# Kernel optimization log

Measured on AMD Instinct MI355X. Metric: run time of the kernel, lower is better.

## Reference

```python
import jax, jax.numpy as jnp
import numpy as np

D_MODEL = 1024
N_HEADS = 16
D_K = D_MODEL // N_HEADS
CAUSAL = True


def setup_inputs() -> dict:
    key = jax.random.key(0)
    ks = jax.random.split(key, 11)
    B, S, D = 2, 2048, D_MODEL
    scale = 1.0 / np.sqrt(D)
    inp = {
        "in_Q": jax.random.normal(ks[0], (B, S, D), jnp.float32),
        "in_K": jax.random.normal(ks[1], (B, S, D), jnp.float32),
        "in_V": jax.random.normal(ks[2], (B, S, D), jnp.float32),
        # torch Linear params: weight [out, in], bias [out]
        "Wq": jax.random.normal(ks[3], (D, D), jnp.float32) * scale,
        "bq": jax.random.normal(ks[4], (D,), jnp.float32) * scale,
        "Wk": jax.random.normal(ks[5], (D, D), jnp.float32) * scale,
        "bk": jax.random.normal(ks[6], (D,), jnp.float32) * scale,
        "Wv": jax.random.normal(ks[7], (D, D), jnp.float32) * scale,
        "bv": jax.random.normal(ks[8], (D,), jnp.float32) * scale,
        "Wo": jax.random.normal(ks[9], (D, D), jnp.float32) * scale,
        "bo": jax.random.normal(ks[10], (D,), jnp.float32) * scale,
    }
    return inp


def reference(in_Q, in_K, in_V, Wq, bq, Wk, bk, Wv, bv, Wo, bo):
    B, S, D = in_Q.shape
    H, dk = N_HEADS, D_K
    # Linear projections (torch: x @ W.T + b)
    Q = in_Q @ Wq.T + bq
    K = in_K @ Wk.T + bk
    V = in_V @ Wv.T + bv
    # split heads: [B, S, D] -> [B, H, S, dk]
    Qh = Q.reshape(B, S, H, dk).transpose(0, 2, 1, 3)
    Kh = K.reshape(B, S, H, dk).transpose(0, 2, 1, 3)
    Vh = V.reshape(B, S, H, dk).transpose(0, 2, 1, 3)
    # scores [B, H, S, S]
    scores = jnp.einsum("bhqd,bhkd->bhqk", Qh, Kh) / jnp.sqrt(jnp.float32(dk))
    if CAUSAL:
        mask = jnp.tril(jnp.ones((S, S), dtype=bool))
        scores = jnp.where(mask, scores, -jnp.inf)
    attn = jax.nn.softmax(scores, axis=-1)
    out = jnp.einsum("bhqk,bhkd->bhqd", attn, Vh)
    Hcat = out.transpose(0, 2, 1, 3).reshape(B, S, D)
    return Hcat @ Wo.T + bo
```

## Files before the change

### kernel.cpp

```cpp
#include <hip/hip_runtime.h>
#include <hip/hip_bf16.h>
#include <math.h>

#define D_MODEL 1024
#define NHEADS  16
#define DK      64
#define SEQ     2048
#define BATCH   2
#define MROWS   4096

typedef unsigned short ushort_t;
using short8 = __attribute__((ext_vector_type(8))) short;
using f32x4  = __attribute__((ext_vector_type(4))) float;

__device__ __forceinline__ ushort_t f2bf(float x) {
    unsigned u = __float_as_uint(x);
    u = (u + 0x7FFFu + ((u >> 16) & 1u)) >> 16;
    return (ushort_t)u;
}

__device__ __forceinline__ unsigned pk2(float a, float b) {
    __hip_bfloat162 h = __float22bfloat162_rn(float2{a, b});
    unsigned u;
    __builtin_memcpy(&u, &h, 4);
    return u;
}

__device__ __forceinline__ void gll16(const ushort_t* g, ushort_t* l) {
    __builtin_amdgcn_global_load_lds(
        (const __attribute__((address_space(1))) void*)(g),
        (__attribute__((address_space(3))) void*)(l), 16, 0, 0);
}

__global__ __launch_bounds__(256) void cvt_bf16(
    const float* s0, const float* s1, const float* s2, const float* s3,
    ushort_t* d0, ushort_t* d1, ushort_t* d2, ushort_t* d3, int n)
{
    const float* s; ushort_t* d;
    switch (blockIdx.y) {
        case 0: s = s0; d = d0; break;
        case 1: s = s1; d = d1; break;
        case 2: s = s2; d = d2; break;
        default: s = s3; d = d3; break;
    }
    int i = (blockIdx.x * 256 + threadIdx.x) * 4;
    if (i < n) {
        float4 v = *(const float4*)&s[i];
        ushort4 o;
        o.x = f2bf(v.x); o.y = f2bf(v.y); o.z = f2bf(v.z); o.w = f2bf(v.w);
        *(ushort4*)&d[i] = o;
    }
}

struct GemmArgs { const ushort_t* A; const ushort_t* W; const float* bias;
                  void* C; int mode; float oscale; };

template<int MODE>
__device__ __forceinline__ void gemm_core(const GemmArgs& ga,
                                          ushort_t* As, ushort_t* Bs)
{
    constexpr bool SWP = (MODE != 1);
    const int tid  = threadIdx.x;
    const int w    = tid >> 6, lane = tid & 63;
    const int quad = lane >> 4, lx = lane & 15;
    const int mw = (w >> 1) * 64, nw = (w & 1) * 64;
    const int bm = blockIdx.x * 128, bn = blockIdx.y * 128;
    const int K = D_MODEL;

    f32x4 acc[4][4];
#pragma unroll
    for (int mt = 0; mt < 4; ++mt)
#pragma unroll
        for (int nt = 0; nt < 4; ++nt)
            acc[mt][nt] = (f32x4){0.f, 0.f, 0.f, 0.f};

    float4 b4[4];
    float  bfr[4];
#pragma unroll
    for (int nt = 0; nt < 4; ++nt) {
        if (SWP) b4[nt] = *(const float4*)&ga.bias[bn + nw + nt * 16 + quad * 4];
        else     bfr[nt] = ga.bias[bn + nw + nt * 16 + lx];
    }

    for (int k0 = 0; k0 < K; k0 += 64) {
        __syncthreads();
#pragma unroll
        for (int i = 0; i < 4; ++i) {
            int r0 = (w * 4 + i) * 8;
            int rl = r0 + (lane >> 3);
            int g  = (lane & 7) ^ (rl & 7);
            gll16(&ga.A[(size_t)(bm + rl) * K + k0 + g * 8], &As[r0 * 64]);
            gll16(&ga.W[(size_t)(bn + rl) * K + k0 + g * 8], &Bs[r0 * 64]);
        }
        __syncthreads();

#pragma unroll
        for (int ks = 0; ks < 2; ++ks) {
            short8 af[4], bf[4];
#pragma unroll
            for (int mt = 0; mt < 4; ++mt) {
                int r = mw + mt * 16 + lx;
                af[mt] = *(const short8*)&As[r * 64 + (((ks * 4 + quad) ^ (r & 7)) << 3)];
            }
#pragma unroll
            for (int nt = 0; nt < 4; ++nt) {
                int r = nw + nt * 16 + lx;
                bf[nt] = *(const short8*)&Bs[r * 64 + (((ks * 4 + quad) ^ (r & 7)) << 3)];
            }
#pragma unroll
            for (int mt = 0; mt < 4; ++mt)
#pragma unroll
                for (int nt = 0; nt < 4; ++nt)
                    acc[mt][nt] = SWP
                        ? __builtin_amdgcn_mfma_f32_16x16x32_bf16(bf[nt], af[mt], acc[mt][nt], 0, 0, 0)
                        : __builtin_amdgcn_mfma_f32_16x16x32_bf16(af[mt], bf[nt], acc[mt][nt], 0, 0, 0);
        }
    }

    if (MODE == 0) {
        ushort_t* C = (ushort_t*)ga.C;
        const float os = ga.oscale;
#pragma unroll
        for (int mt = 0; mt < 4; ++mt) {
            int m = bm + mw + mt * 16 + lx;
#pragma unroll
            for (int nt = 0; nt < 4; ++nt) {
                int n0 = bn + nw + nt * 16 + quad * 4;
                uint2 u;
                u.x = pk2((acc[mt][nt][0] + b4[nt].x) * os, (acc[mt][nt][1] + b4[nt].y) * os);
                u.y = pk2((acc[mt][nt][2] + b4[nt].z) * os, (acc[mt][nt][3] + b4[nt].w) * os);
                *(uint2*)&C[(size_t)m * D_MODEL + n0] = u;
            }
        }
    } else if (MODE == 2) {
        float* C = (float*)ga.C;
#pragma unroll
        for (int mt = 0; mt < 4; ++mt) {
            int m = bm + mw + mt * 16 + lx;
#pragma unroll
            for (int nt = 0; nt < 4; ++nt) {
                int n0 = bn + nw + nt * 16 + quad * 4;
                float4 v;
                v.x = acc[mt][nt][0] + b4[nt].x;
                v.y = acc[mt][nt][1] + b4[nt].y;
                v.z = acc[mt][nt][2] + b4[nt].z;
                v.w = acc[mt][nt][3] + b4[nt].w;
                *(float4*)&C[(size_t)m * D_MODEL + n0] = v;
            }
        }
    } else {
        ushort_t* C = (ushort_t*)ga.C;
#pragma unroll
        for (int mt = 0; mt < 4; ++mt)
#pragma unroll
            for (int nt = 0; nt < 4; ++nt) {
                int n = bn + nw + nt * 16 + lx;
                int d = n & 63, h = n >> 6;
                int m0 = bm + mw + mt * 16 + quad * 4;
                int b = m0 >> 11, s0 = m0 & 2047;
                uint2 u;
                u.x = pk2(acc[mt][nt][0] + bfr[nt], acc[mt][nt][1] + bfr[nt]);
                u.y = pk2(acc[mt][nt][2] + bfr[nt], acc[mt][nt][3] + bfr[nt]);
                *(uint2*)&C[((size_t)(b * NHEADS + h) * DK + d) * SEQ + s0] = u;
            }
    }
}

__global__ __launch_bounds__(256) void gemm_mfma(GemmArgs g0, GemmArgs g1, GemmArgs g2)
{
    __shared__ ushort_t As[128 * 64];
    __shared__ ushort_t Bs[128 * 64];
    GemmArgs ga = (blockIdx.z == 0) ? g0 : ((blockIdx.z == 1) ? g1 : g2);
    if (ga.mode == 0)      gemm_core<0>(ga, As, Bs);
    else if (ga.mode == 1) gemm_core<1>(ga, As, Bs);
    else                   gemm_core<2>(ga, As, Bs);
}

__global__ __launch_bounds__(256) void flash_mfma(
    const ushort_t* __restrict__ Qp, const ushort_t* __restrict__ Kp,
    const ushort_t* __restrict__ Vt, ushort_t* __restrict__ Hc)
{
    const int qt = (int)gridDim.x - 1 - (int)blockIdx.x;
    const int bh = blockIdx.y;
    const int b = bh >> 4, h = bh & 15;
    const int tid  = threadIdx.x;
    const int w    = tid >> 6, lane = tid & 63;
    const int quad = lane >> 4, lx = lane & 15;

    __shared__ ushort_t Ks[64 * 64];
    __shared__ ushort_t Vs[64 * 64];
    __shared__ ushort_t Ps[4][16 * 72];

    const size_t qbase = (size_t)(b * SEQ) * D_MODEL + h * DK;
    const size_t vbase = (size_t)bh * DK * SEQ;

    short8 qf[2];
    {
        size_t ro = qbase + (size_t)(qt * 64 + w * 16 + lx) * D_MODEL + quad * 8;
        qf[0] = *(const short8*)&Qp[ro];
        qf[1] = *(const short8*)&Qp[ro + 32];
    }

    f32x4 O[4];
#pragma unroll
    for (int nt = 0; nt < 4; ++nt) O[nt] = (f32x4){0.f, 0.f, 0.f, 0.f};
    float mrow = -INFINITY, lrow = 0.f;
    const int qin = w * 16 + lx;

    for (int kt = 0; kt <= qt; ++kt) {
        __syncthreads();
#pragma unroll
        for (int i = 0; i < 2; ++i) {
            int r0 = (w + i * 4) * 8;
            int rl = r0 + (lane >> 3);
            int g  = (lane & 7) ^ (rl & 7);
            gll16(&Kp[qbase + (size_t)(kt * 64 + rl) * D_MODEL + g * 8], &Ks[r0 * 64]);
            gll16(&Vt[vbase + (size_t)rl * SEQ + kt * 64 + g * 8], &Vs[r0 * 64]);
        }
        __syncthreads();

        f32x4 s[4];
#pragma unroll
        for (int nt = 0; nt < 4; ++nt) {
            int r = nt * 16 + lx;
            short8 kf0 = *(const short8*)&Ks[r * 64 + ((quad ^ (r & 7)) << 3)];
            short8 kf1 = *(const short8*)&Ks[r * 64 + (((4 + quad) ^ (r & 7)) << 3)];
            f32x4 z = (f32x4){0.f, 0.f, 0.f, 0.f};
            z = __builtin_amdgcn_mfma_f32_16x16x32_bf16(kf0, qf[0], z, 0, 0, 0);
            z = __builtin_amdgcn_mfma_f32_16x16x32_bf16(kf1, qf[1], z, 0, 0, 0);
            s[nt] = z;
        }

        if (kt == qt) {
#pragma unroll
            for (int nt = 0; nt < 4; ++nt)
#pragma unroll
                for (int r = 0; r < 4; ++r)
                    if ((nt * 16 + quad * 4 + r) > qin) s[nt][r] = -INFINITY;
        }

        float tm = -INFINITY;
#pragma unroll
        for (int nt = 0; nt < 4; ++nt)
#pragma unroll
            for (int r = 0; r < 4; ++r) tm = fmaxf(tm, s[nt][r]);
        tm = fmaxf(tm, __shfl_xor(tm, 16, 64));
        tm = fmaxf(tm, __shfl_xor(tm, 32, 64));
        float mnew = fmaxf(mrow, tm);
        float alpha = __builtin_amdgcn_exp2f(mrow - mnew);
        mrow = mnew;
        float rs = 0.f;
#pragma unroll
        for (int nt = 0; nt < 4; ++nt)
#pragma unroll
            for (int r = 0; r < 4; ++r) {
                float p = __builtin_amdgcn_exp2f(s[nt][r] - mnew);
                s[nt][r] = p;
                rs += p;
            }
        rs += __shfl_xor(rs, 16, 64);
        rs += __shfl_xor(rs, 32, 64);
        lrow = lrow * alpha + rs;
#pragma unroll
        for (int nt = 0; nt < 4; ++nt)
#pragma unroll
            for (int r = 0; r < 4; ++r) O[nt][r] *= alpha;

#pragma unroll
        for (int nt = 0; nt < 4; ++nt) {
            uint2 u;
            u.x = pk2(s[nt][0], s[nt][1]);
            u.y = pk2(s[nt][2], s[nt][3]);
            *(uint2*)&Ps[w][lx * 72 + nt * 16 + quad * 4] = u;
        }

        short8 pf0 = *(const short8*)&Ps[w][lx * 72 + quad * 8];
        short8 pf1 = *(const short8*)&Ps[w][lx * 72 + 32 + quad * 8];

#pragma unroll
        for (int nt = 0; nt < 4; ++nt) {
            int r = nt * 16 + lx;
            short8 vf0 = *(const short8*)&Vs[r * 64 + ((quad ^ (r & 7)) << 3)];
            short8 vf1 = *(const short8*)&Vs[r * 64 + (((4 + quad) ^ (r & 7)) << 3)];
            O[nt] = __builtin_amdgcn_mfma_f32_16x16x32_bf16(vf0, pf0, O[nt], 0, 0, 0);
            O[nt] = __builtin_amdgcn_mfma_f32_16x16x32_bf16(vf1, pf1, O[nt], 0, 0, 0);
        }
    }

    {
        float invl = 1.f / lrow;
        size_t ro = qbase + (size_t)(qt * 64 + w * 16 + lx) * D_MODEL;
#pragma unroll
        for (int nt = 0; nt < 4; ++nt) {
            uint2 u;
            u.x = pk2(O[nt][0] * invl, O[nt][1] * invl);
            u.y = pk2(O[nt][2] * invl, O[nt][3] * invl);
            *(uint2*)&Hc[ro + nt * 16 + quad * 4] = u;
        }
    }
}

extern "C" void kernel_launch(void* const* d_in, const int* in_sizes, int n_in,
                              void* d_out, int out_size, void* d_ws, size_t ws_size,
                              hipStream_t stream) {
    const float* inQ = (const float*)d_in[0];
    const float* inK = (const float*)d_in[1];
    const float* inV = (const float*)d_in[2];
    const float* Wq  = (const float*)d_in[3];
    const float* bq  = (const float*)d_in[4];
    const float* Wk  = (const float*)d_in[5];
    const float* bk  = (const float*)d_in[6];
    const float* Wv  = (const float*)d_in[7];
    const float* bv  = (const float*)d_in[8];
    const float* Wo  = (const float*)d_in[9];
    const float* bo  = (const float*)d_in[10];
    float* out = (float*)d_out;

    const size_t NI = (size_t)MROWS * D_MODEL;
    const size_t NW = (size_t)D_MODEL * D_MODEL;
    ushort_t* ws  = (ushort_t*)d_ws;
    ushort_t* Qb  = ws;
    ushort_t* Kb  = Qb  + NI;
    ushort_t* Vb  = Kb  + NI;
    ushort_t* Wqb = Vb  + NI;
    ushort_t* Wkb = Wqb + NW;
    ushort_t* Wvb = Wkb + NW;
    ushort_t* Wob = Wvb + NW;
    ushort_t* Qp  = Wob + NW;
    ushort_t* Kp  = Qp  + NI;
    ushort_t* Vtg = Kp  + NI;
    ushort_t* Hc  = Vtg + NI;

    cvt_bf16<<<dim3(NI / 1024, 3), 256, 0, stream>>>(
        inQ, inK, inV, inV, Qb, Kb, Vb, Vb, (int)NI);
    cvt_bf16<<<dim3(NW / 1024, 4), 256, 0, stream>>>(
        Wq, Wk, Wv, Wo, Wqb, Wkb, Wvb, Wob, (int)NW);

    const float qsc = 0.125f * 1.44269504088896340736f;
    GemmArgs aq{Qb, Wqb, bq, (void*)Qp, 0, qsc};
    GemmArgs ak{Kb, Wkb, bk, (void*)Kp, 0, 1.0f};
    GemmArgs av{Vb, Wvb, bv, (void*)Vtg, 1, 1.0f};
    gemm_mfma<<<dim3(MROWS / 128, D_MODEL / 128, 3), 256, 0, stream>>>(aq, ak, av);

    flash_mfma<<<dim3(SEQ / 64, BATCH * NHEADS), 256, 0, stream>>>(Qp, Kp, Vtg, Hc);

    GemmArgs ao{Hc, Wob, bo, (void*)out, 2, 1.0f};
    gemm_mfma<<<dim3(MROWS / 128, D_MODEL / 128, 1), 256, 0, stream>>>(ao, ao, ao);
}
```

Measured before the change: 261.8 us.

## Pair causal query tiles per flash block and merge conversion launches

Each flash-attention block now handles two query tiles, qt = NQT-1-p and qt = p, so every block does the same total causal work and the grid shrinks to 16x32 blocks. This is meant to remove the load imbalance of triangular causal attention. The cost is fewer blocks (512 on a GPU with many CUs) and serial processing of the two tiles within a block. The two bf16 conversion launches are also merged into one launch with 7 grid rows, which saves a kernel launch; the weight rows exit early past nW, so those blocks are wasted.

```diff
diff --git a/kernel.cpp b/kernel.cpp
--- a/kernel.cpp
+++ b/kernel.cpp
@@ -8,6 +8,7 @@
 #define SEQ     2048
 #define BATCH   2
 #define MROWS   4096
+#define NQT     (SEQ/64)
 
 typedef unsigned short ushort_t;
 using short8 = __attribute__((ext_vector_type(8))) short;
@@ -34,14 +35,19 @@
 
 __global__ __launch_bounds__(256) void cvt_bf16(
     const float* s0, const float* s1, const float* s2, const float* s3,
-    ushort_t* d0, ushort_t* d1, ushort_t* d2, ushort_t* d3, int n)
-{
-    const float* s; ushort_t* d;
+    const float* s4, const float* s5, const float* s6,
+    ushort_t* d0, ushort_t* d1, ushort_t* d2, ushort_t* d3,
+    ushort_t* d4, ushort_t* d5, ushort_t* d6, int nIn, int nW)
+{
+    const float* s; ushort_t* d; int n;
     switch (blockIdx.y) {
-        case 0: s = s0; d = d0; break;
-        case 1: s = s1; d = d1; break;
-        case 2: s = s2; d = d2; break;
-        default: s = s3; d = d3; break;
+        case 0: s = s0; d = d0; n = nIn; break;
+        case 1: s = s1; d = d1; n = nIn; break;
+        case 2: s = s2; d = d2; n = nIn; break;
+        case 3: s = s3; d = d3; n = nW;  break;
+        case 4: s = s4; d = d4; n = nW;  break;
+        case 5: s = s5; d = d5; n = nW;  break;
+        default: s = s6; d = d6; n = nW; break;
     }
     int i = (blockIdx.x * 256 + threadIdx.x) * 4;
     if (i < n) {
@@ -176,23 +182,15 @@
     else                   gemm_core<2>(ga, As, Bs);
 }
 
-__global__ __launch_bounds__(256) void flash_mfma(
+__device__ __forceinline__ void flash_tile(
+    int qt, const size_t qbase, const size_t vbase,
     const ushort_t* __restrict__ Qp, const ushort_t* __restrict__ Kp,
-    const ushort_t* __restrict__ Vt, ushort_t* __restrict__ Hc)
-{
-    const int qt = (int)gridDim.x - 1 - (int)blockIdx.x;
-    const int bh = blockIdx.y;
-    const int b = bh >> 4, h = bh & 15;
+    const ushort_t* __restrict__ Vt, ushort_t* __restrict__ Hc,
+    ushort_t* Ks, ushort_t* Vs, ushort_t (*Ps)[16 * 72])
+{
     const int tid  = threadIdx.x;
     const int w    = tid >> 6, lane = tid & 63;
     const int quad = lane >> 4, lx = lane & 15;
-
-    __shared__ ushort_t Ks[64 * 64];
-    __shared__ ushort_t Vs[64 * 64];
-    __shared__ ushort_t Ps[4][16 * 72];
-
-    const size_t qbase = (size_t)(b * SEQ) * D_MODEL + h * DK;
-    const size_t vbase = (size_t)bh * DK * SEQ;
 
     short8 qf[2];
     {
@@ -298,6 +296,25 @@
             *(uint2*)&Hc[ro + nt * 16 + quad * 4] = u;
         }
     }
+}
+
+__global__ __launch_bounds__(256) void flash_mfma(
+    const ushort_t* __restrict__ Qp, const ushort_t* __restrict__ Kp,
+    const ushort_t* __restrict__ Vt, ushort_t* __restrict__ Hc)
+{
+    const int p  = blockIdx.x;
+    const int bh = blockIdx.y;
+    const int b = bh >> 4, h = bh & 15;
+
+    __shared__ ushort_t Ks[64 * 64];
+    __shared__ ushort_t Vs[64 * 64];
+    __shared__ ushort_t Ps[4][16 * 72];
+
+    const size_t qbase = (size_t)(b * SEQ) * D_MODEL + h * DK;
+    const size_t vbase = (size_t)bh * DK * SEQ;
+
+    flash_tile(NQT - 1 - p, qbase, vbase, Qp, Kp, Vt, Hc, Ks, Vs, Ps);
+    flash_tile(p,           qbase, vbase, Qp, Kp, Vt, Hc, Ks, Vs, Ps);
 }
 
 extern "C" void kernel_launch(void* const* d_in, const int* in_sizes, int n_in,
@@ -331,10 +348,9 @@
     ushort_t* Vtg = Kp  + NI;
     ushort_t* Hc  = Vtg + NI;
 
-    cvt_bf16<<<dim3(NI / 1024, 3), 256, 0, stream>>>(
-        inQ, inK, inV, inV, Qb, Kb, Vb, Vb, (int)NI);
-    cvt_bf16<<<dim3(NW / 1024, 4), 256, 0, stream>>>(
-        Wq, Wk, Wv, Wo, Wqb, Wkb, Wvb, Wob, (int)NW);
+    cvt_bf16<<<dim3(NI / 1024, 7), 256, 0, stream>>>(
+        inQ, inK, inV, Wq, Wk, Wv, Wo,
+        Qb, Kb, Vb, Wqb, Wkb, Wvb, Wob, (int)NI, (int)NW);
 
     const float qsc = 0.125f * 1.44269504088896340736f;
     GemmArgs aq{Qb, Wqb, bq, (void*)Qp, 0, qsc};
@@ -342,7 +358,7 @@
     GemmArgs av{Vb, Wvb, bv, (void*)Vtg, 1, 1.0f};
     gemm_mfma<<<dim3(MROWS / 128, D_MODEL / 128, 3), 256, 0, stream>>>(aq, ak, av);
 
-    flash_mfma<<<dim3(SEQ / 64, BATCH * NHEADS), 256, 0, stream>>>(Qp, Kp, Vtg, Hc);
+    flash_mfma<<<dim3(NQT / 2, BATCH * NHEADS), 256, 0, stream>>>(Qp, Kp, Vtg, Hc);
 
     GemmArgs ao{Hc, Wob, bo, (void*)out, 2, 1.0f};
     gemm_mfma<<<dim3(MROWS / 128, D_MODEL / 128, 1), 256, 0, stream>>>(ao, ao, ao);
```

Measured after the change: 232.2 us. 11.3% less time.
